# Kernel optimization log

Hardware: AMD Instinct MI355X
Metric: run time of the kernel (lower is better)

Reference implementation:

```python
import jax, jax.numpy as jnp
import numpy as np

B = 4        # samples
GP = 6       # graphs per sample (K*2)
N = 1024     # nodes per graph
DIN = 128    # input feature dim
D = 128      # out_channels
E = 16384    # edges per graph


def setup_inputs() -> dict:
    k = jax.random.split(jax.random.key(0), 10)
    G = B * GP
    s = 0.05
    return {
        "x": jax.random.normal(k[0], (G, N, DIN), jnp.float32),
        "edge_attr": jax.random.uniform(k[1], (G, E, 6), jnp.float32),
        "gcn_W": jax.random.normal(k[2], (4, DIN, D), jnp.float32) * s,
        "gcn_b": jnp.zeros((4, D), jnp.float32),
        "Ws": jax.random.normal(k[3], (4, D, D), jnp.float32) * s,
        "lin1_W": jax.random.normal(k[4], (GP * D, 20), jnp.float32) * s,
        "lin1_b": jnp.zeros((20,), jnp.float32),
        "codefc_W": jax.random.normal(k[5], (20, 2), jnp.float32) * s,
        "codefc_b": jnp.zeros((2,), jnp.float32),
        "lin2_W": jax.random.normal(k[6], (GP * D, GP), jnp.float32) * s,
        "lin2_b": jnp.zeros((GP,), jnp.float32),
        "simfc_W": jax.random.normal(k[7], (GP, 2), jnp.float32) * s,
        "simfc_b": jnp.zeros((2,), jnp.float32),
        "edge_index": jax.random.randint(k[8], (G, 2, E), 0, N, jnp.int64),
    }


def _gcn(x, src, dst, ew, W, b):
    # PyG GCNConv with normalize=True, add_self_loops=True (self-loop weight 1)
    n = x.shape[0]
    deg = jax.ops.segment_sum(ew, dst, num_segments=n) + 1.0
    dinv = jax.lax.rsqrt(deg)
    xw = x @ W
    norm = dinv[src] * ew * dinv[dst]               # [E]
    agg = jax.ops.segment_sum(norm[:, None] * xw[src], dst, num_segments=n)
    return agg + (dinv * dinv)[:, None] * xw + b    # self-loop term + bias


def _gnnlayer(x, ei, ea, gcn_W, gcn_b, Ws):
    # x_tmp = sum_i relu(GCN_i(x, ew=edge_attr[:, i+2])) @ Ws[i]
    src, dst = ei[0], ei[1]
    def chan(W, b, Wmix, ew):
        return jnp.maximum(_gcn(x, src, dst, ew, W, b), 0.0) @ Wmix
    return jax.vmap(chan)(gcn_W, gcn_b, Ws, ea[:, 2:6].T).sum(0)  # [N, D]


def _forward(x, edge_attr, gcn_W, gcn_b, Ws, lin1_W, lin1_b, codefc_W,
             codefc_b, lin2_W, lin2_b, simfc_W, simfc_b, edge_index):
    # per-graph GNN layer over all G = B*GP graphs
    x_tmp = jax.vmap(lambda xg, eig, eag: _gnnlayer(xg, eig, eag, gcn_W, gcn_b, Ws))(
        x, edge_index, edge_attr)                    # [G, N, D]
    g = x_tmp.mean(axis=1).reshape(B, GP * D)        # g_matrix [B, 768]
    # L2-normalize rows (F.normalize eps=1e-12)
    xn = x_tmp / jnp.clip(jnp.linalg.norm(x_tmp, axis=-1, keepdims=True), 1e-12)
    xn = xn.reshape(B, GP, N, D)
    # all-pairs cosine sim -> tanh -> 21-bin histogram on [-1, 1] -> weighted sum
    S = jnp.tanh(jnp.einsum('bind,bjmd->bijnm', xn, xn))   # [B,GP,GP,N,N]
    idx = jnp.clip(jnp.floor((S + 1.0) * (21.0 / 2.0)).astype(jnp.int32), 0, 20)
    centers = jnp.linspace(-1.0, 1.0, 21, dtype=jnp.float32)
    # hist/(N*N) dot centers == mean of per-element bin centers
    sim = centers[idx].mean(axis=(3, 4))             # [B, GP, GP]
    # backnet
    feat = jnp.maximum(g @ lin1_W + lin1_b, 0.0)     # feature_of_G [B, 20]
    code = jax.nn.log_softmax(feat @ codefc_W + codefc_b, axis=1)
    strength = g @ lin2_W + lin2_b                   # [B, GP]
    sim_res = jax.nn.log_softmax((sim.mean(axis=2) * strength) @ simfc_W + simfc_b, axis=1)
    r = 0.4 * code + 0.6 * sim_res
    return r, feat


def reference(x, edge_attr, gcn_W, gcn_b, Ws, lin1_W, lin1_b, codefc_W,
              codefc_b, lin2_W, lin2_b, simfc_W, simfc_b, edge_index):
    return _forward(x, edge_attr, gcn_W, gcn_b, Ws, lin1_W, lin1_b, codefc_W,
                    codefc_b, lin2_W, lin2_b, simfc_W, simfc_b, edge_index)
```

## Files before the change

### kernel.cpp

```cpp
#include <hip/hip_runtime.h>

#define NG 24
#define NB 4
#define GPg 6
#define NN 1024
#define DD 128
#define EE 16384

typedef __bf16 bf16;
typedef __bf16 bf16x8 __attribute__((ext_vector_type(8)));
typedef float f32x4 __attribute__((ext_vector_type(4)));

#define GLOBAL_AS __attribute__((address_space(1)))
#define LDS_AS __attribute__((address_space(3)))

__global__ void k_convert(const float* __restrict__ x, const float* __restrict__ gW,
                          const float* __restrict__ Ws, bf16* __restrict__ xb,
                          bf16* __restrict__ gwt, bf16* __restrict__ wst) {
  int i = blockIdx.x * 256 + threadIdx.x;
  if (i < NG * NN * DD) xb[i] = (bf16)x[i];
  if (i < 4 * DD * DD) {
    int c = i >> 14, k = (i >> 7) & 127, j = i & 127;
    gwt[(c << 14) | (j << 7) | k] = (bf16)gW[i];
    wst[(j << 9) | (c << 7) | k] = (bf16)Ws[i];
  }
}

__global__ void k_hist(const int* __restrict__ ei, int* __restrict__ counts) {
  int t = blockIdx.x * 256 + threadIdx.x;
  if (t >= NG * EE) return;
  int g = t >> 14, e = t & (EE - 1);
  int dst = ei[g * 2 * EE + EE + e];
  atomicAdd(&counts[g * NN + dst], 1);
}

__global__ void k_scan(const int* __restrict__ counts, int* __restrict__ offs,
                       int* __restrict__ cursor) {
  __shared__ int sh[NN];
  int g = blockIdx.x, t = threadIdx.x;
  int myc = counts[g * NN + t];
  sh[t] = myc;
  __syncthreads();
  for (int d2 = 1; d2 < NN; d2 <<= 1) {
    int v = (t >= d2) ? sh[t - d2] : 0;
    __syncthreads();
    sh[t] += v;
    __syncthreads();
  }
  int incl = sh[t];
  int excl = incl - myc;
  offs[g * 1025 + t] = excl;
  cursor[g * NN + t] = excl;
  if (t == NN - 1) offs[g * 1025 + NN] = incl;
}

__global__ void k_scatter(const int* __restrict__ ei, const float* __restrict__ ea,
                          int* __restrict__ cursor, int* __restrict__ csrs,
                          float* __restrict__ csre) {
  int t = blockIdx.x * 256 + threadIdx.x;
  if (t >= NG * EE) return;
  int g = t >> 14, e = t & (EE - 1);
  int src = ei[g * 2 * EE + e], dst = ei[g * 2 * EE + EE + e];
  int pos = atomicAdd(&cursor[g * NN + dst], 1);
  size_t idx = (size_t)g * EE + pos;
  csrs[idx] = src;
  const float* p = ea + ((size_t)g * EE + e) * 6;
#pragma unroll
  for (int c = 0; c < 4; c++) csre[idx * 4 + c] = p[2 + c];
}

__global__ void k_deg(const int* __restrict__ offs, const float* __restrict__ csre,
                      float* __restrict__ dinv4) {
  int t = blockIdx.x * 256 + threadIdx.x;
  int c = t & 3, n = (t >> 2) & (NN - 1), g = t >> 12;
  int beg = offs[g * 1025 + n], end = offs[g * 1025 + n + 1];
  const float* ep = csre + (size_t)g * EE * 4 + c;
  float s = 1.0f;
  for (int p = beg; p < end; ++p) s += ep[(size_t)p * 4];
  dinv4[t] = rsqrtf(s);
}

__global__ __launch_bounds__(256) void k_xw(const bf16* __restrict__ xb,
                                            const bf16* __restrict__ gwt,
                                            const float* __restrict__ dinv4,
                                            bf16* __restrict__ xw) {
  int bid = blockIdx.x;
  int gc = bid >> 3, mb = bid & 7;
  int g = gc >> 2, c = gc & 3;
  int lane = threadIdx.x & 63, wid = threadIdx.x >> 6;
  int wm = wid >> 1, wn = wid & 1;
  int row0 = mb * 128 + wm * 64, col0 = wn * 64;
  const bf16* A = xb + (size_t)g * NN * DD;
  const bf16* Bt = gwt + (size_t)c * DD * DD;
  int lr = lane & 15, lk = (lane >> 4) * 8;
  f32x4 acc[4][4] = {};
  for (int kc = 0; kc < 128; kc += 32) {
    bf16x8 a[4], b[4];
#pragma unroll
    for (int i2 = 0; i2 < 4; i2++)
      a[i2] = *(const bf16x8*)(A + (size_t)(row0 + i2 * 16 + lr) * DD + kc + lk);
#pragma unroll
    for (int j2 = 0; j2 < 4; j2++)
      b[j2] = *(const bf16x8*)(Bt + (size_t)(col0 + j2 * 16 + lr) * DD + kc + lk);
#pragma unroll
    for (int i2 = 0; i2 < 4; i2++)
#pragma unroll
      for (int j2 = 0; j2 < 4; j2++)
        acc[i2][j2] = __builtin_amdgcn_mfma_f32_16x16x32_bf16(a[i2], b[j2], acc[i2][j2], 0, 0, 0);
  }
  bf16* out = xw + (size_t)g * NN * 512 + c * 128;
  const float* dv = dinv4 + ((size_t)g * NN) * 4 + c;
  int cr = (lane >> 4) * 4, cc = lane & 15;
#pragma unroll
  for (int i2 = 0; i2 < 4; i2++)
#pragma unroll
    for (int r2 = 0; r2 < 4; r2++) {
      int row = row0 + i2 * 16 + cr + r2;
      float dvv = dv[row * 4];
#pragma unroll
      for (int j2 = 0; j2 < 4; j2++)
        out[(size_t)row * 512 + col0 + j2 * 16 + cc] = (bf16)(acc[i2][j2][r2] * dvv);
    }
}

__global__ __launch_bounds__(256) void k_agg(const int* __restrict__ offs, const int* __restrict__ csrs,
                                             const float* __restrict__ csre, const float* __restrict__ dinv4,
                                             const float* __restrict__ gb, const bf16* __restrict__ xw,
                                             bf16* __restrict__ hb) {
  int bid = blockIdx.x;
  int lb = (bid & 7) * (NG * 256 / 8) + (bid >> 3);
  int g = lb >> 8, n4 = lb & 255;
  int wid = threadIdx.x >> 6, lane = threadIdx.x & 63;
  int n = n4 * 4 + wid;
  int c = lane >> 4, d0 = (lane & 15) * 8;
  const bf16* xwg = xw + (size_t)g * NN * 512;
  int beg = offs[g * 1025 + n], end = offs[g * 1025 + n + 1];
  const int* sp = csrs + (size_t)g * EE;
  const float* ep = csre + (size_t)g * EE * 4;
  float dvn = dinv4[((size_t)g * NN + n) * 4 + c];
  float acc[8] = {};
  int p = beg;
  for (; p + 1 < end; p += 2) {
    int s0 = sp[p], s1 = sp[p + 1];
    float w0 = ep[(size_t)p * 4 + c];
    float w1 = ep[(size_t)(p + 1) * 4 + c];
    bf16x8 v0 = *(const bf16x8*)(xwg + (size_t)s0 * 512 + lane * 8);
    bf16x8 v1 = *(const bf16x8*)(xwg + (size_t)s1 * 512 + lane * 8);
#pragma unroll
    for (int q = 0; q < 8; q++) acc[q] += w0 * (float)v0[q];
#pragma unroll
    for (int q = 0; q < 8; q++) acc[q] += w1 * (float)v1[q];
  }
  if (p < end) {
    int s0 = sp[p];
    float w0 = ep[(size_t)p * 4 + c];
    bf16x8 v0 = *(const bf16x8*)(xwg + (size_t)s0 * 512 + lane * 8);
#pragma unroll
    for (int q = 0; q < 8; q++) acc[q] += w0 * (float)v0[q];
  }
  bf16x8 vs = *(const bf16x8*)(xwg + (size_t)n * 512 + lane * 8);
  bf16x8 o;
#pragma unroll
  for (int q = 0; q < 8; q++) {
    float r2 = dvn * (acc[q] + (float)vs[q]) + gb[c * 128 + d0 + q];
    o[q] = (bf16)fmaxf(r2, 0.f);
  }
  *(bf16x8*)(hb + ((size_t)g * NN + n) * 512 + lane * 8) = o;
}

__global__ __launch_bounds__(256) void k_mixn(const bf16* __restrict__ hb,
                                              const bf16* __restrict__ wst,
                                              float* __restrict__ gmat,
                                              bf16* __restrict__ xn) {
  __shared__ float rowssq[128];
  int bid = blockIdx.x;
  int g = bid >> 3, mb = bid & 7;
  int lane = threadIdx.x & 63, wid = threadIdx.x >> 6;
  int wm = wid >> 1, wn = wid & 1;
  int row0 = mb * 128 + wm * 64, col0 = wn * 64;
  const bf16* H = hb + (size_t)g * NN * 512;
  int lr = lane & 15, lk = (lane >> 4) * 8;
  if (threadIdx.x < 128) rowssq[threadIdx.x] = 0.f;
  f32x4 acc[4][4] = {};
  for (int kc = 0; kc < 512; kc += 32) {
    bf16x8 a[4], b[4];
#pragma unroll
    for (int i2 = 0; i2 < 4; i2++)
      a[i2] = *(const bf16x8*)(H + (size_t)(row0 + i2 * 16 + lr) * 512 + kc + lk);
#pragma unroll
    for (int j2 = 0; j2 < 4; j2++)
      b[j2] = *(const bf16x8*)(wst + (size_t)(col0 + j2 * 16 + lr) * 512 + kc + lk);
#pragma unroll
    for (int i2 = 0; i2 < 4; i2++)
#pragma unroll
      for (int j2 = 0; j2 < 4; j2++)
        acc[i2][j2] = __builtin_amdgcn_mfma_f32_16x16x32_bf16(a[i2], b[j2], acc[i2][j2], 0, 0, 0);
  }
  __syncthreads();
  int cr = (lane >> 4) * 4, cc = lane & 15;
#pragma unroll
  for (int i2 = 0; i2 < 4; i2++)
#pragma unroll
    for (int r2 = 0; r2 < 4; r2++) {
      float s = 0.f;
#pragma unroll
      for (int j2 = 0; j2 < 4; j2++) { float v = acc[i2][j2][r2]; s += v * v; }
#pragma unroll
      for (int d2 = 1; d2 < 16; d2 <<= 1) s += __shfl_xor(s, d2);
      if (cc == 0) atomicAdd(&rowssq[wm * 64 + i2 * 16 + cr + r2], s);
    }
#pragma unroll
  for (int j2 = 0; j2 < 4; j2++) {
    float s = 0.f;
#pragma unroll
    for (int i2 = 0; i2 < 4; i2++)
#pragma unroll
      for (int r2 = 0; r2 < 4; r2++) s += acc[i2][j2][r2];
    s += __shfl_xor(s, 16);
    s += __shfl_xor(s, 32);
    if ((lane >> 4) == 0)
      atomicAdd(&gmat[(g / GPg) * 768 + (g % GPg) * 128 + col0 + j2 * 16 + cc], s * (1.0f / NN));
  }
  __syncthreads();
  bf16* xp = xn + (size_t)g * NN * DD;
#pragma unroll
  for (int i2 = 0; i2 < 4; i2++)
#pragma unroll
    for (int r2 = 0; r2 < 4; r2++) {
      int rowl = wm * 64 + i2 * 16 + cr + r2;
      float inv = 1.0f / fmaxf(sqrtf(rowssq[rowl]), 1e-12f);
#pragma unroll
      for (int j2 = 0; j2 < 4; j2++)
        xp[(size_t)(mb * 128 + rowl) * DD + col0 + j2 * 16 + cc] = (bf16)(acc[i2][j2][r2] * inv);
    }
}

__global__ __launch_bounds__(256, 4) void k_pair(const bf16* __restrict__ xn,
                                                 unsigned* __restrict__ simsum) {
  __shared__ char lds[32768];
  int bid = blockIdx.x;
  int lb = (bid & 7) * 168 + (bid >> 3);
  int b = lb / 336, rem = lb % 336;
  int pj = rem >> 4, rs = rem & 15;
  int r = pj, i = 0;
  while (r >= 6 - i) { r -= 6 - i; ++i; }
  int j = i + r;
  bool isdiag = (i == j);
  int t0 = isdiag ? rs : 0;
  int lane = threadIdx.x & 63, wid = threadIdx.x >> 6;
  int lr = lane & 15, hk16 = (lane >> 4) * 16;
  const bf16* Ag = xn + ((size_t)(b * GPg + i) * NN + rs * 64 + wid * 16) * DD;
  const char* Bg0 = (const char*)(xn + (size_t)(b * GPg + j) * NN * DD);

  bf16x8 a[4];
#pragma unroll
  for (int kc = 0; kc < 4; kc++)
    a[kc] = *(const bf16x8*)((const char*)Ag + lr * 256 + kc * 64 + hk16);

  auto stage = [&](int buf, int tn) {
    const char* src = Bg0 + tn * 16384;
#pragma unroll
    for (int u = 0; u < 4; ++u) {
      int o = u * 4096 + wid * 1024 + lane * 16;
      int so = o ^ (((o >> 8) & 7) << 4);
      __builtin_amdgcn_global_load_lds((const GLOBAL_AS void*)(src + so),
                                       (LDS_AS void*)(lds + buf * 16384 + o), 16, 0, 0);
    }
  };
  stage(0, t0);
  if (t0 + 1 < 16) stage(1, t0 + 1);

  int cnt = 0;
  int cc = lane & 15, cr = (lane >> 4) * 4;
  for (int t = t0; t < 16; ++t) {
    int cur = (t - t0) & 1;
    if (t < 15) asm volatile("s_waitcnt vmcnt(4)" ::: "memory");
    else        asm volatile("s_waitcnt vmcnt(0)" ::: "memory");
    __builtin_amdgcn_s_barrier();
    const char* Bl = lds + cur * 16384;
    f32x4 acc[4] = {};
#pragma unroll
    for (int kc = 0; kc < 4; kc++) {
      bf16x8 bb[4];
#pragma unroll
      for (int j2 = 0; j2 < 4; j2++) {
        int lrow = j2 * 16 + lr;
        int byte = lrow * 256 + ((kc * 64 + hk16) ^ ((lrow & 7) << 4));
        bb[j2] = *(const bf16x8*)(Bl + byte);
      }
#pragma unroll
      for (int j2 = 0; j2 < 4; j2++)
        acc[j2] = __builtin_amdgcn_mfma_f32_16x16x32_bf16(a[kc], bb[j2], acc[j2], 0, 0, 0);
    }
    asm volatile("s_waitcnt lgkmcnt(0)" ::: "memory");
    __builtin_amdgcn_sched_barrier(0);
    __builtin_amdgcn_s_barrier();
    if (t + 2 < 16) stage(cur, t + 2);
    if (isdiag && t == rs) {
      int tc = 0;
#pragma unroll
      for (int j2 = 0; j2 < 4; j2++)
#pragma unroll
        for (int r2 = 0; r2 < 4; r2++) {
          float v = acc[j2][r2];
          float e = __builtin_amdgcn_exp2f(v * 2.8853900817779268f);
          float wv = 21.f - 21.f * __builtin_amdgcn_rcpf(e + 1.f);
          int idx = (int)fminf(wv, 20.f);
          int lm = j2 * 16 + cc, ln = wid * 16 + cr + r2;
          tc += (lm > ln) ? 2 * idx : (lm == ln ? idx : 0);
        }
      cnt += tc;
    } else {
      int tc = 0;
#pragma unroll
      for (int j2 = 0; j2 < 4; j2++)
#pragma unroll
        for (int r2 = 0; r2 < 4; r2++) {
          float v = acc[j2][r2];
          float e = __builtin_amdgcn_exp2f(v * 2.8853900817779268f);
          float wv = 21.f - 21.f * __builtin_amdgcn_rcpf(e + 1.f);
          tc += (int)fminf(wv, 20.f);
        }
      cnt += isdiag ? 2 * tc : tc;
    }
  }
#pragma unroll
  for (int d2 = 32; d2; d2 >>= 1) cnt += __shfl_xor(cnt, d2);
  if (lane == 0) atomicAdd(&simsum[((size_t)b * GPg + i) * GPg + j], (unsigned)cnt);
}

__global__ void k_back(const float* __restrict__ gmat, const unsigned* __restrict__ simsum,
                       const float* __restrict__ l1W, const float* __restrict__ l1b,
                       const float* __restrict__ cfW, const float* __restrict__ cfb,
                       const float* __restrict__ l2W, const float* __restrict__ l2b,
                       const float* __restrict__ sfW, const float* __restrict__ sfb,
                       float* __restrict__ out) {
  __shared__ float feat[NB][20];
  __shared__ float strength[NB][GPg];
  __shared__ float simmean[NB][GPg];
  int t = threadIdx.x;
  if (t < 80) {
    int b = t / 20, jj = t % 20;
    float s = l1b[jj];
    for (int k = 0; k < 768; k++) s += gmat[b * 768 + k] * l1W[k * 20 + jj];
    float f = fmaxf(s, 0.f);
    feat[b][jj] = f;
    out[8 + b * 20 + jj] = f;
  } else if (t < 104) {
    int q = t - 80; int b = q / GPg, pp = q % GPg;
    float s = l2b[pp];
    for (int k = 0; k < 768; k++) s += gmat[b * 768 + k] * l2W[k * GPg + pp];
    strength[b][pp] = s;
  } else if (t < 128) {
    int q = t - 104; int b = q / GPg, ii = q % GPg;
    float s = 0.f;
    for (int jj = 0; jj < GPg; jj++) {
      int lo = ii < jj ? ii : jj, hi = ii < jj ? jj : ii;
      s += -1.0f + 0.1f * (float)simsum[(b * GPg + lo) * GPg + hi] * (1.0f / (1024.f * 1024.f));
    }
    simmean[b][ii] = s * (1.0f / GPg);
  }
  __syncthreads();
  if (t < NB) {
    int b = t;
    float l1v[2], l2v[2];
#pragma unroll
    for (int u = 0; u < 2; u++) {
      float s = cfb[u];
      for (int jj = 0; jj < 20; jj++) s += feat[b][jj] * cfW[jj * 2 + u];
      l1v[u] = s;
      float s2 = sfb[u];
      for (int pp = 0; pp < GPg; pp++) s2 += simmean[b][pp] * strength[b][pp] * sfW[pp * 2 + u];
      l2v[u] = s2;
    }
    float m1 = fmaxf(l1v[0], l1v[1]);
    float lse1 = m1 + logf(expf(l1v[0] - m1) + expf(l1v[1] - m1));
    float m2 = fmaxf(l2v[0], l2v[1]);
    float lse2 = m2 + logf(expf(l2v[0] - m2) + expf(l2v[1] - m2));
    out[b * 2 + 0] = 0.4f * (l1v[0] - lse1) + 0.6f * (l2v[0] - lse2);
    out[b * 2 + 1] = 0.4f * (l1v[1] - lse1) + 0.6f * (l2v[1] - lse2);
  }
}

extern "C" void kernel_launch(void* const* d_in, const int* in_sizes, int n_in,
                              void* d_out, int out_size, void* d_ws, size_t ws_size,
                              hipStream_t stream) {
  const float* x   = (const float*)d_in[0];
  const float* ea  = (const float*)d_in[1];
  const float* gW  = (const float*)d_in[2];
  const float* gb  = (const float*)d_in[3];
  const float* Ws  = (const float*)d_in[4];
  const float* l1W = (const float*)d_in[5];
  const float* l1b = (const float*)d_in[6];
  const float* cfW = (const float*)d_in[7];
  const float* cfb = (const float*)d_in[8];
  const float* l2W = (const float*)d_in[9];
  const float* l2b = (const float*)d_in[10];
  const float* sfW = (const float*)d_in[11];
  const float* sfb = (const float*)d_in[12];
  const int* eidx  = (const int*)d_in[13];
  float* out = (float*)d_out;

  char* w = (char*)d_ws;
  auto alloc = [&](size_t bytes) { char* p = w; w += (bytes + 255) & ~(size_t)255; return (void*)p; };
  bf16* xb      = (bf16*)alloc((size_t)NG * NN * DD * 2);
  bf16* gwt     = (bf16*)alloc(4 * DD * DD * 2);
  bf16* wst     = (bf16*)alloc(4 * DD * DD * 2);
  int* counts   = (int*)alloc((size_t)NG * NN * 4);
  float* dinv4  = (float*)alloc((size_t)NG * NN * 4 * 4);
  int* offs     = (int*)alloc((size_t)NG * 1025 * 4);
  int* cursor   = (int*)alloc((size_t)NG * NN * 4);
  int* csrs     = (int*)alloc((size_t)NG * EE * 4);
  float* csre   = (float*)alloc((size_t)NG * EE * 4 * 4);
  bf16* xw      = (bf16*)alloc((size_t)NG * NN * 512 * 2);
  bf16* hb      = (bf16*)alloc((size_t)NG * NN * 512 * 2);
  float* gmat   = (float*)alloc((size_t)NB * 768 * 4);
  unsigned* simsum = (unsigned*)alloc((size_t)NB * 36 * 4);
  bf16* xn      = (bf16*)alloc((size_t)NG * NN * DD * 2 + 16384);

  hipMemsetAsync(counts, 0, (size_t)NG * NN * 4, stream);
  hipMemsetAsync(gmat, 0, 12288 + 576, stream);

  k_convert<<<(NG * NN * DD) / 256, 256, 0, stream>>>(x, gW, Ws, xb, gwt, wst);
  k_hist<<<(NG * EE) / 256, 256, 0, stream>>>(eidx, counts);
  k_scan<<<NG, 1024, 0, stream>>>(counts, offs, cursor);
  k_scatter<<<(NG * EE) / 256, 256, 0, stream>>>(eidx, ea, cursor, csrs, csre);
  k_deg<<<(NG * NN * 4) / 256, 256, 0, stream>>>(offs, csre, dinv4);
  k_xw<<<NG * 4 * 8, 256, 0, stream>>>(xb, gwt, dinv4, xw);
  k_agg<<<NG * 256, 256, 0, stream>>>(offs, csrs, csre, dinv4, gb, xw, hb);
  k_mixn<<<NG * 8, 256, 0, stream>>>(hb, wst, gmat, xn);
  k_pair<<<1344, 256, 0, stream>>>(xn, simsum);
  k_back<<<1, 128, 0, stream>>>(gmat, simsum, l1W, l1b, cfW, cfb, l2W, l2b, sfW, sfb, out);
}
```

Before: 205.5 us.

## Double per-block row tile in pair kernel, remap LDS layout, parallelize backnet

The pairwise similarity kernel now gives each block 128 rows of graph i instead of 64, with each wave holding two 16-row A fragments. Every B tile loaded into LDS is reused for twice as many MFMAs, and half as many blocks are launched. The LDS staging now writes B in an MFMA-fragment-ordered layout, so the XOR swizzle is gone and fragments are read linearly. The diagonal masking is updated to the larger tile, and the fminf clamp before the histogram bin is dropped. The small backnet kernel splits each 768-long dot product across 8 lanes with shuffle reductions and launches 1024 threads; the cost is fewer blocks for latency hiding and more registers per thread in the pair kernel.

```diff
diff --git a/kernel.cpp b/kernel.cpp
--- a/kernel.cpp
+++ b/kernel.cpp
@@ -239,33 +239,36 @@
                                                  unsigned* __restrict__ simsum) {
   __shared__ char lds[32768];
   int bid = blockIdx.x;
-  int lb = (bid & 7) * 168 + (bid >> 3);
-  int b = lb / 336, rem = lb % 336;
-  int pj = rem >> 4, rs = rem & 15;
+  int lb = (bid & 7) * 84 + (bid >> 3);
+  int b = lb / 168, rem = lb % 168;
+  int pj = rem >> 3, s128 = rem & 7;
   int r = pj, i = 0;
   while (r >= 6 - i) { r -= 6 - i; ++i; }
   int j = i + r;
   bool isdiag = (i == j);
-  int t0 = isdiag ? rs : 0;
+  int t0 = isdiag ? 2 * s128 : 0;
   int lane = threadIdx.x & 63, wid = threadIdx.x >> 6;
-  int lr = lane & 15, hk16 = (lane >> 4) * 16;
-  const bf16* Ag = xn + ((size_t)(b * GPg + i) * NN + rs * 64 + wid * 16) * DD;
+  int lr = lane & 15, hi16 = (lane >> 4) * 16;
+  const char* Ag = (const char*)(xn + ((size_t)(b * GPg + i) * NN + s128 * 128 + wid * 32) * DD);
   const char* Bg0 = (const char*)(xn + (size_t)(b * GPg + j) * NN * DD);
 
-  bf16x8 a[4];
-#pragma unroll
-  for (int kc = 0; kc < 4; kc++)
-    a[kc] = *(const bf16x8*)((const char*)Ag + lr * 256 + kc * 64 + hk16);
-
+  bf16x8 a[2][4];
+#pragma unroll
+  for (int g2 = 0; g2 < 2; g2++)
+#pragma unroll
+    for (int kc = 0; kc < 4; kc++) {
+      a[g2][kc] = *(const bf16x8*)(Ag + (g2 * 16 + lr) * 256 + kc * 64 + hi16);
+      asm volatile("" :: "v"(a[g2][kc]));
+    }
+
+  int gofs = (wid * 16 + lr) * 256 + hi16;
   auto stage = [&](int buf, int tn) {
-    const char* src = Bg0 + tn * 16384;
-#pragma unroll
-    for (int u = 0; u < 4; ++u) {
-      int o = u * 4096 + wid * 1024 + lane * 16;
-      int so = o ^ (((o >> 8) & 7) << 4);
-      __builtin_amdgcn_global_load_lds((const GLOBAL_AS void*)(src + so),
-                                       (LDS_AS void*)(lds + buf * 16384 + o), 16, 0, 0);
-    }
+    const char* src = Bg0 + tn * 16384 + gofs;
+#pragma unroll
+    for (int u = 0; u < 4; ++u)
+      __builtin_amdgcn_global_load_lds((const GLOBAL_AS void*)(src + u * 64),
+                                       (LDS_AS void*)(lds + buf * 16384 + u * 4096 + wid * 1024),
+                                       16, 0, 0);
   };
   stage(0, t0);
   if (t0 + 1 < 16) stage(1, t0 + 1);
@@ -278,49 +281,51 @@
     else        asm volatile("s_waitcnt vmcnt(0)" ::: "memory");
     __builtin_amdgcn_s_barrier();
     const char* Bl = lds + cur * 16384;
-    f32x4 acc[4] = {};
+    f32x4 acc[2][4] = {};
 #pragma unroll
     for (int kc = 0; kc < 4; kc++) {
       bf16x8 bb[4];
 #pragma unroll
-      for (int j2 = 0; j2 < 4; j2++) {
-        int lrow = j2 * 16 + lr;
-        int byte = lrow * 256 + ((kc * 64 + hk16) ^ ((lrow & 7) << 4));
-        bb[j2] = *(const bf16x8*)(Bl + byte);
-      }
-#pragma unroll
       for (int j2 = 0; j2 < 4; j2++)
-        acc[j2] = __builtin_amdgcn_mfma_f32_16x16x32_bf16(a[kc], bb[j2], acc[j2], 0, 0, 0);
+        bb[j2] = *(const bf16x8*)(Bl + kc * 4096 + j2 * 1024 + lane * 16);
+#pragma unroll
+      for (int g2 = 0; g2 < 2; g2++)
+#pragma unroll
+        for (int j2 = 0; j2 < 4; j2++)
+          acc[g2][j2] = __builtin_amdgcn_mfma_f32_16x16x32_bf16(a[g2][kc], bb[j2], acc[g2][j2], 0, 0, 0);
     }
     asm volatile("s_waitcnt lgkmcnt(0)" ::: "memory");
     __builtin_amdgcn_sched_barrier(0);
     __builtin_amdgcn_s_barrier();
     if (t + 2 < 16) stage(cur, t + 2);
-    if (isdiag && t == rs) {
+    if (isdiag && t < t0 + 2) {
       int tc = 0;
 #pragma unroll
-      for (int j2 = 0; j2 < 4; j2++)
-#pragma unroll
-        for (int r2 = 0; r2 < 4; r2++) {
-          float v = acc[j2][r2];
-          float e = __builtin_amdgcn_exp2f(v * 2.8853900817779268f);
-          float wv = 21.f - 21.f * __builtin_amdgcn_rcpf(e + 1.f);
-          int idx = (int)fminf(wv, 20.f);
-          int lm = j2 * 16 + cc, ln = wid * 16 + cr + r2;
-          tc += (lm > ln) ? 2 * idx : (lm == ln ? idx : 0);
-        }
+      for (int g2 = 0; g2 < 2; g2++)
+#pragma unroll
+        for (int j2 = 0; j2 < 4; j2++)
+#pragma unroll
+          for (int r2 = 0; r2 < 4; r2++) {
+            float v = acc[g2][j2][r2];
+            float e = __builtin_amdgcn_exp2f(v * 2.8853900817779268f);
+            int idx = (int)(21.f - 21.f * __builtin_amdgcn_rcpf(e + 1.f));
+            int lm = t * 64 + j2 * 16 + cc;
+            int ln = s128 * 128 + wid * 32 + g2 * 16 + cr + r2;
+            tc += (lm > ln) ? 2 * idx : (lm == ln ? idx : 0);
+          }
       cnt += tc;
     } else {
       int tc = 0;
 #pragma unroll
-      for (int j2 = 0; j2 < 4; j2++)
-#pragma unroll
-        for (int r2 = 0; r2 < 4; r2++) {
-          float v = acc[j2][r2];
-          float e = __builtin_amdgcn_exp2f(v * 2.8853900817779268f);
-          float wv = 21.f - 21.f * __builtin_amdgcn_rcpf(e + 1.f);
-          tc += (int)fminf(wv, 20.f);
-        }
+      for (int g2 = 0; g2 < 2; g2++)
+#pragma unroll
+        for (int j2 = 0; j2 < 4; j2++)
+#pragma unroll
+          for (int r2 = 0; r2 < 4; r2++) {
+            float v = acc[g2][j2][r2];
+            float e = __builtin_amdgcn_exp2f(v * 2.8853900817779268f);
+            tc += (int)(21.f - 21.f * __builtin_amdgcn_rcpf(e + 1.f));
+          }
       cnt += isdiag ? 2 * tc : tc;
     }
   }
@@ -338,21 +343,27 @@
   __shared__ float feat[NB][20];
   __shared__ float strength[NB][GPg];
   __shared__ float simmean[NB][GPg];
-  int t = threadIdx.x;
-  if (t < 80) {
-    int b = t / 20, jj = t % 20;
-    float s = l1b[jj];
-    for (int k = 0; k < 768; k++) s += gmat[b * 768 + k] * l1W[k * 20 + jj];
-    float f = fmaxf(s, 0.f);
-    feat[b][jj] = f;
-    out[8 + b * 20 + jj] = f;
-  } else if (t < 104) {
-    int q = t - 80; int b = q / GPg, pp = q % GPg;
-    float s = l2b[pp];
-    for (int k = 0; k < 768; k++) s += gmat[b * 768 + k] * l2W[k * GPg + pp];
-    strength[b][pp] = s;
-  } else if (t < 128) {
-    int q = t - 104; int b = q / GPg, ii = q % GPg;
+  int t = threadIdx.x, g = t >> 3, l = t & 7;
+  if (g < 80) {
+    int b = g / 20, jj = g % 20;
+    float s = 0.f;
+#pragma unroll 8
+    for (int k = l; k < 768; k += 8) s += gmat[b * 768 + k] * l1W[k * 20 + jj];
+    s += __shfl_xor(s, 1); s += __shfl_xor(s, 2); s += __shfl_xor(s, 4);
+    if (l == 0) {
+      float f = fmaxf(s + l1b[jj], 0.f);
+      feat[b][jj] = f;
+      out[8 + b * 20 + jj] = f;
+    }
+  } else if (g < 104) {
+    int q = g - 80, b = q / GPg, pp = q % GPg;
+    float s = 0.f;
+#pragma unroll 8
+    for (int k = l; k < 768; k += 8) s += gmat[b * 768 + k] * l2W[k * GPg + pp];
+    s += __shfl_xor(s, 1); s += __shfl_xor(s, 2); s += __shfl_xor(s, 4);
+    if (l == 0) strength[b][pp] = s + l2b[pp];
+  } else if (t >= 832 && t < 856) {
+    int q = t - 832; int b = q / GPg, ii = q % GPg;
     float s = 0.f;
     for (int jj = 0; jj < GPg; jj++) {
       int lo = ii < jj ? ii : jj, hi = ii < jj ? jj : ii;
@@ -429,6 +440,6 @@
   k_xw<<<NG * 4 * 8, 256, 0, stream>>>(xb, gwt, dinv4, xw);
   k_agg<<<NG * 256, 256, 0, stream>>>(offs, csrs, csre, dinv4, gb, xw, hb);
   k_mixn<<<NG * 8, 256, 0, stream>>>(hb, wst, gmat, xn);
-  k_pair<<<1344, 256, 0, stream>>>(xn, simsum);
-  k_back<<<1, 128, 0, stream>>>(gmat, simsum, l1W, l1b, cfW, cfb, l2W, l2b, sfW, sfb, out);
-}
+  k_pair<<<672, 256, 0, stream>>>(xn, simsum);
+  k_back<<<1, 1024, 0, stream>>>(gmat, simsum, l1W, l1b, cfW, cfb, l2W, l2b, sfW, sfb, out);
+}
```

Measured after the change: 186.6 us. 9.2% less time.
